# Kernel tuning notes

Measured on AMD Instinct MI355X. Metric: run time of the kernel, lower is better.

## Reference

```python
import math
import jax, jax.numpy as jnp
import numpy as np

M = 0.4
H = 0.333
S = 64.0
T_ALPHA = 1.0
EPS = 1e-3
BM0 = 20.0   # initial batch_mean buffer
BS0 = 100.0  # initial batch_std buffer


def setup_inputs() -> dict:
    key = jax.random.key(0)
    k1, k2, k3 = jax.random.split(key, 3)
    N, C = 2048, 50000
    cosine = jax.random.uniform(k1, (N, C), dtype=jnp.float32)  # in [0,1) subset of valid cosine range
    norms = jax.random.uniform(k2, (N, 1), dtype=jnp.float32)
    label = jax.random.randint(k3, (N,), 0, C, dtype=jnp.int64)
    return {"cosine": cosine, "norms": norms, "label": label}


def reference(cosine, norms, label):
    N, C = cosine.shape
    valid = (label != -1)                      # rows that get a margin (partial-FC)
    validf = valid.astype(cosine.dtype)

    # norm statistics are detached in the original (clone().detach())
    safe_norms = jax.lax.stop_gradient(jnp.clip(norms, 1e-3, 100.0))
    mean = safe_norms.mean()
    std = jnp.std(safe_norms, ddof=1)          # torch .std() is unbiased
    batch_mean = mean * T_ALPHA + (1.0 - T_ALPHA) * BM0
    batch_std = std * T_ALPHA + (1.0 - T_ALPHA) * BS0

    margin_scaler = jnp.clip((safe_norms - batch_mean) / (batch_std + EPS) * H, -1.0, 1.0)[:, 0]  # [N]

    rows = jnp.arange(N)
    lab = jnp.where(valid, label, 0)

    # angular margin: add g_angular at the label column, then clip full positive rows
    theta = jnp.arccos(cosine)                 # [N, C]
    g_angular = -M * margin_scaler * validf    # [N]
    theta = theta.at[rows, lab].add(g_angular)
    theta = jnp.where(valid[:, None], jnp.clip(theta, EPS, math.pi - EPS), theta)
    cos_m = jnp.cos(theta)

    # additive margin at the label column
    g_add = (M + M * margin_scaler) * validf   # [N]
    cos_m = cos_m.at[rows, lab].add(-g_add)

    return cos_m * S
```

## Files before the change

kernel.cpp:

```cpp
#include <hip/hip_runtime.h>
#include <math.h>


#define MARGIN    0.4f
#define HPARAM    0.333f
#define SCALE     64.0f
#define EPSF      1e-3f
#define COS_EPS   0.999999500000041653f
#define PI_M_EPS  3.140592653589793f

typedef float f32x4 __attribute__((ext_vector_type(4)));

__device__ __forceinline__ f32x4 clipscale(f32x4 x) {
    f32x4 y;
    y.x = fminf(fmaxf(x.x, -COS_EPS), COS_EPS) * SCALE;
    y.y = fminf(fmaxf(x.y, -COS_EPS), COS_EPS) * SCALE;
    y.z = fminf(fmaxf(x.z, -COS_EPS), COS_EPS) * SCALE;
    y.w = fminf(fmaxf(x.w, -COS_EPS), COS_EPS) * SCALE;
    return y;
}

__global__ __launch_bounds__(256) void adaface_fused(
        const float* __restrict__ cosine,
        const float* __restrict__ norms,
        const int*   __restrict__ label,
        float*       __restrict__ out,
        int N, int C, int C4) {
    const int t   = threadIdx.x;
    const int row = blockIdx.x;
    const int lab = label[row];

    const f32x4* __restrict__ src = reinterpret_cast<const f32x4*>(cosine) + (size_t)row * (size_t)C4;
    f32x4*       __restrict__ dst = reinterpret_cast<f32x4*>(out)          + (size_t)row * (size_t)C4;

    if (lab != -1) {
        __shared__ double sdata[256];
        double s = 0.0;
        for (int i = t; i < N; i += 256)
            s += (double)fminf(fmaxf(norms[i], 1e-3f), 100.0f);
        sdata[t] = s;
        __syncthreads();
        for (int k = 128; k > 0; k >>= 1) {
            if (t < k) sdata[t] += sdata[t + k];
            __syncthreads();
        }
        const double mean = sdata[0] / (double)N;
        __syncthreads();
        double sq = 0.0;
        for (int i = t; i < N; i += 256) {
            double d = (double)fminf(fmaxf(norms[i], 1e-3f), 100.0f) - mean;
            sq += d * d;
        }
        sdata[t] = sq;
        __syncthreads();
        for (int k = 128; k > 0; k >>= 1) {
            if (t < k) sdata[t] += sdata[t + k];
            __syncthreads();
        }
        const float bm = (float)mean;
        const float bs = (float)sqrt(sdata[0] / (double)(N - 1));

        const int lab4 = lab >> 2;
        const int labk = lab & 3;
        float fix = 0.0f;
        if (t == (lab4 & 255)) {
            const float sn = fminf(fmaxf(norms[row], 1e-3f), 100.0f);
            const float ms = fminf(fmaxf((sn - bm) / (bs + EPSF) * HPARAM, -1.0f), 1.0f);
            const float xv = cosine[(size_t)row * (size_t)C + (size_t)lab];
            float theta = acosf(xv) - MARGIN * ms;
            theta = fminf(fmaxf(theta, EPSF), PI_M_EPS);
            fix = (cosf(theta) - (MARGIN + MARGIN * ms)) * SCALE;
        }

        int c4 = t;
        for (; c4 + 256 < C4; c4 += 512) {
            f32x4 x0 = src[c4];
            f32x4 x1 = src[c4 + 256];
            f32x4 y0 = clipscale(x0);
            f32x4 y1 = clipscale(x1);
            if (c4 == lab4) {
                y0.x = (labk == 0) ? fix : y0.x;
                y0.y = (labk == 1) ? fix : y0.y;
                y0.z = (labk == 2) ? fix : y0.z;
                y0.w = (labk == 3) ? fix : y0.w;
            }
            if (c4 + 256 == lab4) {
                y1.x = (labk == 0) ? fix : y1.x;
                y1.y = (labk == 1) ? fix : y1.y;
                y1.z = (labk == 2) ? fix : y1.z;
                y1.w = (labk == 3) ? fix : y1.w;
            }
            dst[c4]       = y0;
            dst[c4 + 256] = y1;
        }
        for (; c4 < C4; c4 += 256) {
            f32x4 y = clipscale(src[c4]);
            if (c4 == lab4) {
                y.x = (labk == 0) ? fix : y.x;
                y.y = (labk == 1) ? fix : y.y;
                y.z = (labk == 2) ? fix : y.z;
                y.w = (labk == 3) ? fix : y.w;
            }
            dst[c4] = y;
        }
    } else {
        int c4 = t;
        for (; c4 + 256 < C4; c4 += 512) {
            f32x4 x0 = src[c4];
            f32x4 x1 = src[c4 + 256];
            f32x4 y0 = { x0.x * SCALE, x0.y * SCALE, x0.z * SCALE, x0.w * SCALE };
            f32x4 y1 = { x1.x * SCALE, x1.y * SCALE, x1.z * SCALE, x1.w * SCALE };
            dst[c4]       = y0;
            dst[c4 + 256] = y1;
        }
        for (; c4 < C4; c4 += 256) {
            f32x4 x = src[c4];
            f32x4 y = { x.x * SCALE, x.y * SCALE, x.z * SCALE, x.w * SCALE };
            dst[c4] = y;
        }
    }
}

extern "C" void kernel_launch(void* const* d_in, const int* in_sizes, int n_in,
                              void* d_out, int out_size, void* d_ws, size_t ws_size,
                              hipStream_t stream) {
    const float* cosine = (const float*)d_in[0];
    const float* norms  = (const float*)d_in[1];
    const int*   label  = (const int*)d_in[2];
    float*       out    = (float*)d_out;

    const int N  = in_sizes[2];
    const int C  = in_sizes[0] / N;
    const int C4 = C / 4;

    adaface_fused<<<N, 256, 0, stream>>>(cosine, norms, label, out, N, C, C4);
}
```

Baseline: 184.3 us.

## Process multiple rows per block, unroll by eight, use nontemporal stores

Each block now handles eight rows, so the norm mean/std reduction runs once per block instead of once per row. The column loop is unrolled to eight float4 loads in flight, and stores use nontemporal hints to avoid polluting cache with streaming output. In exchange the grid shrinks to 256 blocks, which leaves little slack for latency hiding or load balance across the device's compute units.

```diff
diff --git a/kernel.cpp b/kernel.cpp
--- a/kernel.cpp
+++ b/kernel.cpp
@@ -8,6 +8,7 @@
 #define EPSF      1e-3f
 #define COS_EPS   0.999999500000041653f
 #define PI_M_EPS  3.140592653589793f
+#define RPB       8
 
 typedef float f32x4 __attribute__((ext_vector_type(4)));
 
@@ -26,97 +27,125 @@
         const int*   __restrict__ label,
         float*       __restrict__ out,
         int N, int C, int C4) {
-    const int t   = threadIdx.x;
-    const int row = blockIdx.x;
-    const int lab = label[row];
+    const int t = threadIdx.x;
 
-    const f32x4* __restrict__ src = reinterpret_cast<const f32x4*>(cosine) + (size_t)row * (size_t)C4;
-    f32x4*       __restrict__ dst = reinterpret_cast<f32x4*>(out)          + (size_t)row * (size_t)C4;
+    __shared__ double sdata[256];
+    double s = 0.0;
+    for (int i = t; i < N; i += 256)
+        s += (double)fminf(fmaxf(norms[i], 1e-3f), 100.0f);
+    sdata[t] = s;
+    __syncthreads();
+    for (int k = 128; k > 0; k >>= 1) {
+        if (t < k) sdata[t] += sdata[t + k];
+        __syncthreads();
+    }
+    const double mean = sdata[0] / (double)N;
+    __syncthreads();
+    double sq = 0.0;
+    for (int i = t; i < N; i += 256) {
+        double d = (double)fminf(fmaxf(norms[i], 1e-3f), 100.0f) - mean;
+        sq += d * d;
+    }
+    sdata[t] = sq;
+    __syncthreads();
+    for (int k = 128; k > 0; k >>= 1) {
+        if (t < k) sdata[t] += sdata[t + k];
+        __syncthreads();
+    }
+    const float bm = (float)mean;
+    const float bs = (float)sqrt(sdata[0] / (double)(N - 1));
 
-    if (lab != -1) {
-        __shared__ double sdata[256];
-        double s = 0.0;
-        for (int i = t; i < N; i += 256)
-            s += (double)fminf(fmaxf(norms[i], 1e-3f), 100.0f);
-        sdata[t] = s;
-        __syncthreads();
-        for (int k = 128; k > 0; k >>= 1) {
-            if (t < k) sdata[t] += sdata[t + k];
-            __syncthreads();
-        }
-        const double mean = sdata[0] / (double)N;
-        __syncthreads();
-        double sq = 0.0;
-        for (int i = t; i < N; i += 256) {
-            double d = (double)fminf(fmaxf(norms[i], 1e-3f), 100.0f) - mean;
-            sq += d * d;
-        }
-        sdata[t] = sq;
-        __syncthreads();
-        for (int k = 128; k > 0; k >>= 1) {
-            if (t < k) sdata[t] += sdata[t + k];
-            __syncthreads();
-        }
-        const float bm = (float)mean;
-        const float bs = (float)sqrt(sdata[0] / (double)(N - 1));
+    const int row0 = blockIdx.x * RPB;
+    for (int r = 0; r < RPB; ++r) {
+        const int row = row0 + r;
+        if (row >= N) break;
+        const int lab = label[row];
+        const f32x4* __restrict__ src = reinterpret_cast<const f32x4*>(cosine) + (size_t)row * (size_t)C4;
+        f32x4*       __restrict__ dst = reinterpret_cast<f32x4*>(out)          + (size_t)row * (size_t)C4;
 
-        const int lab4 = lab >> 2;
-        const int labk = lab & 3;
-        float fix = 0.0f;
-        if (t == (lab4 & 255)) {
+        if (lab != -1) {
+            const int lab4 = lab >> 2;
+            const int labk = lab & 3;
             const float sn = fminf(fmaxf(norms[row], 1e-3f), 100.0f);
             const float ms = fminf(fmaxf((sn - bm) / (bs + EPSF) * HPARAM, -1.0f), 1.0f);
-            const float xv = cosine[(size_t)row * (size_t)C + (size_t)lab];
-            float theta = acosf(xv) - MARGIN * ms;
+            float theta = acosf(cosine[(size_t)row * (size_t)C + (size_t)lab]) - MARGIN * ms;
             theta = fminf(fmaxf(theta, EPSF), PI_M_EPS);
-            fix = (cosf(theta) - (MARGIN + MARGIN * ms)) * SCALE;
-        }
+            const float fix = (cosf(theta) - (MARGIN + MARGIN * ms)) * SCALE;
 
-        int c4 = t;
-        for (; c4 + 256 < C4; c4 += 512) {
-            f32x4 x0 = src[c4];
-            f32x4 x1 = src[c4 + 256];
-            f32x4 y0 = clipscale(x0);
-            f32x4 y1 = clipscale(x1);
-            if (c4 == lab4) {
-                y0.x = (labk == 0) ? fix : y0.x;
-                y0.y = (labk == 1) ? fix : y0.y;
-                y0.z = (labk == 2) ? fix : y0.z;
-                y0.w = (labk == 3) ? fix : y0.w;
+            int c4 = t;
+            for (; c4 + 7 * 256 < C4; c4 += 8 * 256) {
+                f32x4 x0 = src[c4];
+                f32x4 x1 = src[c4 + 1 * 256];
+                f32x4 x2 = src[c4 + 2 * 256];
+                f32x4 x3 = src[c4 + 3 * 256];
+                f32x4 x4 = src[c4 + 4 * 256];
+                f32x4 x5 = src[c4 + 5 * 256];
+                f32x4 x6 = src[c4 + 6 * 256];
+                f32x4 x7 = src[c4 + 7 * 256];
+                f32x4 y0 = clipscale(x0), y1 = clipscale(x1), y2 = clipscale(x2), y3 = clipscale(x3);
+                f32x4 y4 = clipscale(x4), y5 = clipscale(x5), y6 = clipscale(x6), y7 = clipscale(x7);
+                if (lab4 >= c4 && lab4 <= c4 + 7 * 256 && ((lab4 - c4) & 255) == 0) {
+                    f32x4* yp = (lab4 - c4 == 0) ? &y0 : (lab4 - c4 == 256) ? &y1 :
+                                (lab4 - c4 == 512) ? &y2 : (lab4 - c4 == 768) ? &y3 :
+                                (lab4 - c4 == 1024) ? &y4 : (lab4 - c4 == 1280) ? &y5 :
+                                (lab4 - c4 == 1536) ? &y6 : &y7;
+                    yp->x = (labk == 0) ? fix : yp->x;
+                    yp->y = (labk == 1) ? fix : yp->y;
+                    yp->z = (labk == 2) ? fix : yp->z;
+                    yp->w = (labk == 3) ? fix : yp->w;
+                }
+                __builtin_nontemporal_store(y0, dst + c4);
+                __builtin_nontemporal_store(y1, dst + c4 + 1 * 256);
+                __builtin_nontemporal_store(y2, dst + c4 + 2 * 256);
+                __builtin_nontemporal_store(y3, dst + c4 + 3 * 256);
+                __builtin_nontemporal_store(y4, dst + c4 + 4 * 256);
+                __builtin_nontemporal_store(y5, dst + c4 + 5 * 256);
+                __builtin_nontemporal_store(y6, dst + c4 + 6 * 256);
+                __builtin_nontemporal_store(y7, dst + c4 + 7 * 256);
             }
-            if (c4 + 256 == lab4) {
-                y1.x = (labk == 0) ? fix : y1.x;
-                y1.y = (labk == 1) ? fix : y1.y;
-                y1.z = (labk == 2) ? fix : y1.z;
-                y1.w = (labk == 3) ? fix : y1.w;
+            for (; c4 < C4; c4 += 256) {
+                f32x4 y = clipscale(src[c4]);
+                if (c4 == lab4) {
+                    y.x = (labk == 0) ? fix : y.x;
+                    y.y = (labk == 1) ? fix : y.y;
+                    y.z = (labk == 2) ? fix : y.z;
+                    y.w = (labk == 3) ? fix : y.w;
+                }
+                __builtin_nontemporal_store(y, dst + c4);
             }
-            dst[c4]       = y0;
-            dst[c4 + 256] = y1;
-        }
-        for (; c4 < C4; c4 += 256) {
-            f32x4 y = clipscale(src[c4]);
-            if (c4 == lab4) {
-                y.x = (labk == 0) ? fix : y.x;
-                y.y = (labk == 1) ? fix : y.y;
-                y.z = (labk == 2) ? fix : y.z;
-                y.w = (labk == 3) ? fix : y.w;
+        } else {
+            int c4 = t;
+            for (; c4 + 7 * 256 < C4; c4 += 8 * 256) {
+                f32x4 x0 = src[c4];
+                f32x4 x1 = src[c4 + 1 * 256];
+                f32x4 x2 = src[c4 + 2 * 256];
+                f32x4 x3 = src[c4 + 3 * 256];
+                f32x4 x4 = src[c4 + 4 * 256];
+                f32x4 x5 = src[c4 + 5 * 256];
+                f32x4 x6 = src[c4 + 6 * 256];
+                f32x4 x7 = src[c4 + 7 * 256];
+                f32x4 y0 = { x0.x * SCALE, x0.y * SCALE, x0.z * SCALE, x0.w * SCALE };
+                f32x4 y1 = { x1.x * SCALE, x1.y * SCALE, x1.z * SCALE, x1.w * SCALE };
+                f32x4 y2 = { x2.x * SCALE, x2.y * SCALE, x2.z * SCALE, x2.w * SCALE };
+                f32x4 y3 = { x3.x * SCALE, x3.y * SCALE, x3.z * SCALE, x3.w * SCALE };
+                f32x4 y4 = { x4.x * SCALE, x4.y * SCALE, x4.z * SCALE, x4.w * SCALE };
+                f32x4 y5 = { x5.x * SCALE, x5.y * SCALE, x5.z * SCALE, x5.w * SCALE };
+                f32x4 y6 = { x6.x * SCALE, x6.y * SCALE, x6.z * SCALE, x6.w * SCALE };
+                f32x4 y7 = { x7.x * SCALE, x7.y * SCALE, x7.z * SCALE, x7.w * SCALE };
+                __builtin_nontemporal_store(y0, dst + c4);
+                __builtin_nontemporal_store(y1, dst + c4 + 1 * 256);
+                __builtin_nontemporal_store(y2, dst + c4 + 2 * 256);
+                __builtin_nontemporal_store(y3, dst + c4 + 3 * 256);
+                __builtin_nontemporal_store(y4, dst + c4 + 4 * 256);
+                __builtin_nontemporal_store(y5, dst + c4 + 5 * 256);
+                __builtin_nontemporal_store(y6, dst + c4 + 6 * 256);
+                __builtin_nontemporal_store(y7, dst + c4 + 7 * 256);
             }
-            dst[c4] = y;
-        }
-    } else {
-        int c4 = t;
-        for (; c4 + 256 < C4; c4 += 512) {
-            f32x4 x0 = src[c4];
-            f32x4 x1 = src[c4 + 256];
-            f32x4 y0 = { x0.x * SCALE, x0.y * SCALE, x0.z * SCALE, x0.w * SCALE };
-            f32x4 y1 = { x1.x * SCALE, x1.y * SCALE, x1.z * SCALE, x1.w * SCALE };
-            dst[c4]       = y0;
-            dst[c4 + 256] = y1;
-        }
-        for (; c4 < C4; c4 += 256) {
-            f32x4 x = src[c4];
-            f32x4 y = { x.x * SCALE, x.y * SCALE, x.z * SCALE, x.w * SCALE };
-            dst[c4] = y;
+            for (; c4 < C4; c4 += 256) {
+                f32x4 x = src[c4];
+                f32x4 y = { x.x * SCALE, x.y * SCALE, x.z * SCALE, x.w * SCALE };
+                __builtin_nontemporal_store(y, dst + c4);
+            }
         }
     }
 }
@@ -133,5 +162,6 @@
     const int C  = in_sizes[0] / N;
     const int C4 = C / 4;
 
-    adaface_fused<<<N, 256, 0, stream>>>(cosine, norms, label, out, N, C, C4);
+    const int grid = (N + RPB - 1) / RPB;
+    adaface_fused<<<grid, 256, 0, stream>>>(cosine, norms, label, out, N, C, C4);
 }
```

Result: no change. 186.8 us (+1.4%).
